# Optimization experiments

Measured on AMD Instinct MI355X. Metric: run time of the kernel, lower is better.

## Reference

```python
import jax, jax.numpy as jnp
import numpy as np

B, N, DIM, H, KVAL = 16, 1024, 128, 8, 4  # b divisible by K*K=16; mask batch = B//(K*K)=1


def setup_inputs() -> dict:
    key = jax.random.key(0)
    ks = jax.random.split(key, 6)
    x = jax.random.normal(ks[0], (B, N, DIM), jnp.float32)
    mask = (jax.random.uniform(ks[1], (B // (KVAL * KVAL), N - 1)) < 0.9).astype(jnp.float32)
    maps = (jax.random.uniform(ks[2], (B, N - 1)) < 0.9).astype(jnp.float32)
    Wqkv = jax.random.normal(ks[3], (DIM, 3 * DIM), jnp.float32) / np.sqrt(DIM)
    Wout = jax.random.normal(ks[4], (DIM, DIM), jnp.float32) / np.sqrt(DIM)
    bout = jnp.zeros((DIM,), jnp.float32)
    return {"x": x, "mask": mask, "maps": maps, "Wqkv": Wqkv, "Wout": Wout,
            "bout": bout, "K": KVAL}


def reference(x, mask, maps, Wqkv, Wout, bout, K):
    b, n, dim = x.shape
    h = H
    d = dim // h
    scale = dim ** -0.5
    qkv = x @ Wqkv                                  # [b, n, 3*dim]
    q, k, v = jnp.split(qkv, 3, axis=-1)

    def to_heads(t):
        return t.reshape(b, n, h, d).transpose(0, 2, 1, 3)  # [b, h, n, d]

    q, k, v = to_heads(q), to_heads(k), to_heads(v)
    dots = jnp.einsum('bhid,bhjd->bhij', q, k) * scale      # [b, h, n, n]
    mask_value = -jnp.finfo(dots.dtype).max

    # block mask: pad first key position with 1, broadcast over K*K batch block
    kk = K * K
    m = jnp.pad(mask, ((0, 0), (1, 0)), constant_values=1.0)  # [b//kk, n]
    dots = dots.reshape(b // kk, kk, h, n, n)
    m5 = m[:, None, None, None, :]
    dots = dots * m5 + mask_value * (1.0 - m5)
    dots = dots.reshape(b, h, n, n)

    # map mask: boolean fill per batch element
    mp = jnp.pad(maps, ((0, 0), (1, 0)), constant_values=1.0)  # [b, n]
    dots = jnp.where(mp[:, None, None, :] != 0, dots, mask_value)

    attn = jax.nn.softmax(dots, axis=-1)
    out = jnp.einsum('bhij,bhjd->bhid', attn, v)            # [b, h, n, d]
    out = out.transpose(0, 2, 1, 3).reshape(b, n, dim)      # [b, n, dim]
    return out @ Wout + bout
```

## Files before the change

### kernel.cpp

```cpp
#include <hip/hip_runtime.h>
#include <math.h>

#define B_   16
#define N_   1024
#define DIM_ 128
#define H_   8
#define D_   16
#define BH_  128

typedef unsigned short u16;
typedef unsigned int   u32;
typedef __attribute__((ext_vector_type(8))) short short8;
typedef __attribute__((ext_vector_type(4))) float f32x4;

__device__ __forceinline__ u16 f2bf(float f) {
    union { float f; u32 i; } c; c.f = f;
    u32 r = c.i + 0x7FFFu + ((c.i >> 16) & 1u);
    return (u16)(r >> 16);
}
__device__ __forceinline__ u32 pack2bf(float a, float b) {
    union { float f; u32 i; } ca, cb; ca.f = a; cb.f = b;
    return ((ca.i + 0x8000u) >> 16) | ((cb.i + 0x8000u) & 0xFFFF0000u);
}
union frag8 { short8 s; u32 w[4]; };

#define BF_ONE  ((short)0x3F80)
#define BF_NINF ((u16)0xFF80)
#define SCALE_L2E (0.08838834764831845f * 1.4426950408889634f)
#define MFMA16 __builtin_amdgcn_mfma_f32_16x16x32_bf16

__global__ __launch_bounds__(256) void qkv_kernel(
    const float* __restrict__ x, const float* __restrict__ Wqkv,
    const float* __restrict__ maskp, const float* __restrict__ mapsp,
    u16* __restrict__ qws, u16* __restrict__ kws2, u16* __restrict__ vtws)
{
    const int tid  = threadIdx.x;
    const int wave = tid >> 6, lane = tid & 63;
    const int i16  = lane & 15, quad = lane >> 4;
    const int cb   = blockIdx.x % 6;
    const int rb   = blockIdx.x / 6;
    const int row_m = rb * 64 + wave * 16;

    const float* xp = x + (size_t)(row_m + i16) * 128;

    short8 a0, a1, a2, a3;
    #define LOADA(A, K0) { \
        const int k0 = (K0) + quad * 8; \
        const float4 xa = *(const float4*)(xp + k0); \
        const float4 xb2 = *(const float4*)(xp + k0 + 4); \
        frag8 t_; \
        t_.w[0] = pack2bf(xa.x, xa.y);  t_.w[1] = pack2bf(xa.z, xa.w); \
        t_.w[2] = pack2bf(xb2.x, xb2.y); t_.w[3] = pack2bf(xb2.z, xb2.w); \
        A = t_.s; }
    LOADA(a0, 0) LOADA(a1, 32) LOADA(a2, 64) LOADA(a3, 96)
    #undef LOADA

    f32x4 acc0 = {0,0,0,0}, acc1 = {0,0,0,0}, acc2 = {0,0,0,0}, acc3 = {0,0,0,0};

    #define KSTEP(A, K0) { \
        const int k0 = (K0) + quad * 8; \
        const float* wk = Wqkv + (size_t)k0 * 384 + cb * 64 + i16; \
        _Pragma("unroll") \
        for (int ct = 0; ct < 4; ct++) { \
            const float* wp = wk + ct * 16; \
            const float w0 = wp[0*384], w1 = wp[1*384], w2 = wp[2*384], w3 = wp[3*384]; \
            const float w4 = wp[4*384], w5 = wp[5*384], w6 = wp[6*384], w7 = wp[7*384]; \
            frag8 b_; \
            b_.w[0] = pack2bf(w0, w1); b_.w[1] = pack2bf(w2, w3); \
            b_.w[2] = pack2bf(w4, w5); b_.w[3] = pack2bf(w6, w7); \
            if      (ct == 0) acc0 = MFMA16(A, b_.s, acc0, 0, 0, 0); \
            else if (ct == 1) acc1 = MFMA16(A, b_.s, acc1, 0, 0, 0); \
            else if (ct == 2) acc2 = MFMA16(A, b_.s, acc2, 0, 0, 0); \
            else              acc3 = MFMA16(A, b_.s, acc3, 0, 0, 0); \
        } }
    KSTEP(a0, 0) KSTEP(a1, 32) KSTEP(a2, 64) KSTEP(a3, 96)
    #undef KSTEP

    const int which = (cb * 64) >> 7;
    const int row   = row_m + quad * 4;
    const int bb    = row >> 10, n = row & 1023;

    #define STORE_CT(CT, ACC) { \
        const int c  = (cb * 64 + CT * 16) & 127; \
        const int h  = c >> 4; \
        const int bh = bb * 8 + h; \
        const int dd = i16; \
        if (which == 0) { \
            u16* p = qws + ((size_t)(bh * N_ + n)) * 16 + dd; \
            p[0]  = f2bf(ACC[0] * SCALE_L2E); p[16] = f2bf(ACC[1] * SCALE_L2E); \
            p[32] = f2bf(ACC[2] * SCALE_L2E); p[48] = f2bf(ACC[3] * SCALE_L2E); \
        } else if (which == 1) { \
            u16* p = kws2 + ((size_t)(bh * N_ + n)) * 32 + dd; \
            p[0]  = f2bf(ACC[0]); p[32] = f2bf(ACC[1]); \
            p[64] = f2bf(ACC[2]); p[96] = f2bf(ACC[3]); \
            if (dd == 0) { \
                _Pragma("unroll") \
                for (int r = 0; r < 4; r++) { \
                    const int nr = n + r; \
                    const bool valid = (nr == 0) || \
                        (maskp[nr - 1] != 0.0f && mapsp[bb * (N_ - 1) + nr - 1] != 0.0f); \
                    kws2[((size_t)(bh * N_ + nr)) * 32 + 16] = valid ? (u16)0 : BF_NINF; \
                } \
            } \
        } else { \
            *(ushort4*)(vtws + ((size_t)(bh * 16 + dd)) * N_ + n) = \
                make_ushort4(f2bf(ACC[0]), f2bf(ACC[1]), f2bf(ACC[2]), f2bf(ACC[3])); \
        } }
    STORE_CT(0, acc0)
    STORE_CT(1, acc1)
    STORE_CT(2, acc2)
    STORE_CT(3, acc3)
    #undef STORE_CT
}

__global__ __launch_bounds__(256) void attn_kernel(
    const u16* __restrict__ qws, const u16* __restrict__ kws2, const u16* __restrict__ vtws,
    u16* __restrict__ attn)
{
    const int tid  = threadIdx.x;
    const int wave = tid >> 6, lane = tid & 63;
    const int i16  = lane & 15, quad = lane >> 4;
    const int bh   = blockIdx.x;
    const int qb   = blockIdx.y;
    const int bb   = bh >> 3, h = bh & 7;
    const int qrow0 = qb * 256 + wave * 64;
    const int perm = ((i16 & 12) << 1) | (i16 & 3);

    const short8 zero8 = {0,0,0,0,0,0,0,0};
    const short8 ones8 = {BF_ONE,BF_ONE,BF_ONE,BF_ONE,BF_ONE,BF_ONE,BF_ONE,BF_ONE};

    short8 qf0 = zero8, qf1 = zero8, qf2 = zero8, qf3 = zero8;
    if (lane < 32) {
        const u16* qp = qws + ((size_t)(bh * N_ + qrow0 + i16)) * 16 + quad * 8;
        qf0 = *(const short8*)(qp);
        qf1 = *(const short8*)(qp + 256);
        qf2 = *(const short8*)(qp + 512);
        qf3 = *(const short8*)(qp + 768);
    } else if (lane < 48) {
        qf0[0] = BF_ONE; qf1[0] = BF_ONE; qf2[0] = BF_ONE; qf3[0] = BF_ONE;
    }

    const u16* kpA = kws2 + ((size_t)(bh * N_ + perm)) * 32 + quad * 8;
    const u16* kpB = kpA + 4 * 32;
    const u16* vp  = vtws + ((size_t)(bh * 16 + i16)) * N_ + quad * 8;

    f32x4 o0 = {0,0,0,0}, o1 = {0,0,0,0}, o2 = {0,0,0,0}, o3 = {0,0,0,0};
    f32x4 l0 = {0,0,0,0}, l1 = {0,0,0,0}, l2 = {0,0,0,0}, l3 = {0,0,0,0};
    const f32x4 zc = {0.f, 0.f, 0.f, 0.f};

    #pragma unroll 2
    for (int j0 = 0; j0 < N_; j0 += 32) {
        const short8 kfA = *(const short8*)kpA;
        const short8 kfB = *(const short8*)kpB;
        const short8 vf  = *(const short8*)vp;
        kpA += 32 * 32; kpB += 32 * 32; vp += 32;

        #define TILE(QF, O, L) { \
            f32x4 stA = MFMA16(kfA, QF, zc, 0, 0, 0); \
            f32x4 stB = MFMA16(kfB, QF, zc, 0, 0, 0); \
            float pA0 = __builtin_amdgcn_exp2f(stA[0]); \
            float pA1 = __builtin_amdgcn_exp2f(stA[1]); \
            float pA2 = __builtin_amdgcn_exp2f(stA[2]); \
            float pA3 = __builtin_amdgcn_exp2f(stA[3]); \
            float pB0 = __builtin_amdgcn_exp2f(stB[0]); \
            float pB1 = __builtin_amdgcn_exp2f(stB[1]); \
            float pB2 = __builtin_amdgcn_exp2f(stB[2]); \
            float pB3 = __builtin_amdgcn_exp2f(stB[3]); \
            frag8 pk; \
            pk.w[0] = pack2bf(pA0, pA1); pk.w[1] = pack2bf(pA2, pA3); \
            pk.w[2] = pack2bf(pB0, pB1); pk.w[3] = pack2bf(pB2, pB3); \
            O = MFMA16(vf,    pk.s, O, 0, 0, 0); \
            L = MFMA16(ones8, pk.s, L, 0, 0, 0); }
        TILE(qf0, o0, l0)
        TILE(qf1, o1, l1)
        TILE(qf2, o2, l2)
        TILE(qf3, o3, l3)
        #undef TILE
    }

    #define OUT_T(T, O, L) { \
        const float inv = 1.0f / L[0]; \
        ushort4 pko = make_ushort4(f2bf(O[0] * inv), f2bf(O[1] * inv), \
                                   f2bf(O[2] * inv), f2bf(O[3] * inv)); \
        *(ushort4*)(attn + ((size_t)(bb * N_ + qrow0 + T * 16 + i16)) * DIM_ \
                    + h * 16 + quad * 4) = pko; }
    OUT_T(0, o0, l0)
    OUT_T(1, o1, l1)
    OUT_T(2, o2, l2)
    OUT_T(3, o3, l3)
    #undef OUT_T
}

__global__ __launch_bounds__(256) void out_kernel(
    const u16* __restrict__ attnw, const float* __restrict__ Wout,
    const float* __restrict__ boutp, float* __restrict__ outp)
{
    const int tid  = threadIdx.x;
    const int wave = tid >> 6, lane = tid & 63;
    const int i16  = lane & 15, quad = lane >> 4;
    const int cb   = blockIdx.x & 1;
    const int rb   = blockIdx.x >> 1;
    const int row_m = rb * 64 + wave * 16;

    const u16* ap = attnw + (size_t)(row_m + i16) * 128;

    f32x4 acc0 = {0,0,0,0}, acc1 = {0,0,0,0}, acc2 = {0,0,0,0}, acc3 = {0,0,0,0};

    #pragma unroll
    for (int ks = 0; ks < 4; ks++) {
        const int k0 = ks * 32 + quad * 8;
        const short8 a = *(const short8*)(ap + k0);
        const float* wk = Wout + (size_t)k0 * 128 + cb * 64 + i16;
        #pragma unroll
        for (int ct = 0; ct < 4; ct++) {
            const float* wp = wk + ct * 16;
            const float w0 = wp[0*128], w1 = wp[1*128], w2 = wp[2*128], w3 = wp[3*128];
            const float w4 = wp[4*128], w5 = wp[5*128], w6 = wp[6*128], w7 = wp[7*128];
            frag8 b_;
            b_.w[0] = pack2bf(w0, w1); b_.w[1] = pack2bf(w2, w3);
            b_.w[2] = pack2bf(w4, w5); b_.w[3] = pack2bf(w6, w7);
            if      (ct == 0) acc0 = MFMA16(a, b_.s, acc0, 0, 0, 0);
            else if (ct == 1) acc1 = MFMA16(a, b_.s, acc1, 0, 0, 0);
            else if (ct == 2) acc2 = MFMA16(a, b_.s, acc2, 0, 0, 0);
            else              acc3 = MFMA16(a, b_.s, acc3, 0, 0, 0);
        }
    }

    const int row = row_m + quad * 4;
    #define STORE_CT(CT, ACC) { \
        const int col = cb * 64 + CT * 16 + i16; \
        const float bo = boutp[col]; \
        float* op = outp + (size_t)row * 128 + col; \
        op[0 * 128] = ACC[0] + bo; \
        op[1 * 128] = ACC[1] + bo; \
        op[2 * 128] = ACC[2] + bo; \
        op[3 * 128] = ACC[3] + bo; }
    STORE_CT(0, acc0)
    STORE_CT(1, acc1)
    STORE_CT(2, acc2)
    STORE_CT(3, acc3)
    #undef STORE_CT
}

extern "C" void kernel_launch(void* const* d_in, const int* in_sizes, int n_in,
                              void* d_out, int out_size, void* d_ws, size_t ws_size,
                              hipStream_t stream) {
    const float* x    = (const float*)d_in[0];
    const float* mask = (const float*)d_in[1];
    const float* maps = (const float*)d_in[2];
    const float* Wqkv = (const float*)d_in[3];
    const float* Wout = (const float*)d_in[4];
    const float* bout = (const float*)d_in[5];
    u16* qws   = (u16*)d_ws;
    u16* kws2  = qws  + (size_t)2 * 1024 * 1024;
    u16* vtws  = kws2 + (size_t)4 * 1024 * 1024;
    u16* attnw = vtws + (size_t)2 * 1024 * 1024;

    qkv_kernel<<<dim3(1536), dim3(256), 0, stream>>>(x, Wqkv, mask, maps, qws, kws2, vtws);
    attn_kernel<<<dim3(128, 4), dim3(256), 0, stream>>>(qws, kws2, vtws, attnw);
    out_kernel<<<dim3(512), dim3(256), 0, stream>>>(attnw, Wout, bout, (float*)d_out);
}
```

Baseline: 129.0 us.

## Stage bf16 weight tiles in LDS for QKV and output projections

Both projection kernels now have the block cooperatively load fp32 weights once, convert them to bf16, and store them transposed in padded shared memory. Each wave then reads its MFMA B-fragments with vector LDS loads, replacing eight strided scalar global loads and packing per fragment in every wave. The QKV kernel also makes each block cover three 64-column tiles instead of one, so a loaded x fragment is reused across more outputs and the grid shrinks from 1536 to 512 blocks. This costs a larger LDS footprint (about 52 KB in qkv) and a barrier, which may reduce occupancy and parallelism.

```diff
diff --git a/kernel.cpp b/kernel.cpp
--- a/kernel.cpp
+++ b/kernel.cpp
@@ -29,20 +29,38 @@
 #define SCALE_L2E (0.08838834764831845f * 1.4426950408889634f)
 #define MFMA16 __builtin_amdgcn_mfma_f32_16x16x32_bf16
 
+#define WSTRIDE 136
+
 __global__ __launch_bounds__(256) void qkv_kernel(
     const float* __restrict__ x, const float* __restrict__ Wqkv,
     const float* __restrict__ maskp, const float* __restrict__ mapsp,
     u16* __restrict__ qws, u16* __restrict__ kws2, u16* __restrict__ vtws)
 {
+    __shared__ u16 wlds[3 * 64 * WSTRIDE];
     const int tid  = threadIdx.x;
     const int wave = tid >> 6, lane = tid & 63;
     const int i16  = lane & 15, quad = lane >> 4;
-    const int cb   = blockIdx.x % 6;
-    const int rb   = blockIdx.x / 6;
+    const int half = blockIdx.x & 1;
+    const int rb   = blockIdx.x >> 1;
     const int row_m = rb * 64 + wave * 16;
+    const int colbase0 = half * 192;
+
+    {
+        const int col = tid & 63, pg = tid >> 6;
+        for (int ci = 0; ci < 3; ci++) {
+            const float* wsrc = Wqkv + colbase0 + ci * 64 + col;
+            u16* dst = wlds + ci * (64 * WSTRIDE) + col * WSTRIDE;
+            #pragma unroll
+            for (int it = 0; it < 16; it++) {
+                const int p = it * 4 + pg;
+                const float v0 = wsrc[(size_t)(2 * p)     * 384];
+                const float v1 = wsrc[(size_t)(2 * p + 1) * 384];
+                *(u32*)(dst + 2 * p) = pack2bf(v0, v1);
+            }
+        }
+    }
 
     const float* xp = x + (size_t)(row_m + i16) * 128;
-
     short8 a0, a1, a2, a3;
     #define LOADA(A, K0) { \
         const int k0 = (K0) + quad * 8; \
@@ -55,62 +73,59 @@
     LOADA(a0, 0) LOADA(a1, 32) LOADA(a2, 64) LOADA(a3, 96)
     #undef LOADA
 
-    f32x4 acc0 = {0,0,0,0}, acc1 = {0,0,0,0}, acc2 = {0,0,0,0}, acc3 = {0,0,0,0};
-
-    #define KSTEP(A, K0) { \
-        const int k0 = (K0) + quad * 8; \
-        const float* wk = Wqkv + (size_t)k0 * 384 + cb * 64 + i16; \
-        _Pragma("unroll") \
-        for (int ct = 0; ct < 4; ct++) { \
-            const float* wp = wk + ct * 16; \
-            const float w0 = wp[0*384], w1 = wp[1*384], w2 = wp[2*384], w3 = wp[3*384]; \
-            const float w4 = wp[4*384], w5 = wp[5*384], w6 = wp[6*384], w7 = wp[7*384]; \
-            frag8 b_; \
-            b_.w[0] = pack2bf(w0, w1); b_.w[1] = pack2bf(w2, w3); \
-            b_.w[2] = pack2bf(w4, w5); b_.w[3] = pack2bf(w6, w7); \
-            if      (ct == 0) acc0 = MFMA16(A, b_.s, acc0, 0, 0, 0); \
-            else if (ct == 1) acc1 = MFMA16(A, b_.s, acc1, 0, 0, 0); \
-            else if (ct == 2) acc2 = MFMA16(A, b_.s, acc2, 0, 0, 0); \
-            else              acc3 = MFMA16(A, b_.s, acc3, 0, 0, 0); \
-        } }
-    KSTEP(a0, 0) KSTEP(a1, 32) KSTEP(a2, 64) KSTEP(a3, 96)
-    #undef KSTEP
-
-    const int which = (cb * 64) >> 7;
-    const int row   = row_m + quad * 4;
-    const int bb    = row >> 10, n = row & 1023;
-
-    #define STORE_CT(CT, ACC) { \
-        const int c  = (cb * 64 + CT * 16) & 127; \
-        const int h  = c >> 4; \
-        const int bh = bb * 8 + h; \
-        const int dd = i16; \
-        if (which == 0) { \
-            u16* p = qws + ((size_t)(bh * N_ + n)) * 16 + dd; \
-            p[0]  = f2bf(ACC[0] * SCALE_L2E); p[16] = f2bf(ACC[1] * SCALE_L2E); \
-            p[32] = f2bf(ACC[2] * SCALE_L2E); p[48] = f2bf(ACC[3] * SCALE_L2E); \
-        } else if (which == 1) { \
-            u16* p = kws2 + ((size_t)(bh * N_ + n)) * 32 + dd; \
-            p[0]  = f2bf(ACC[0]); p[32] = f2bf(ACC[1]); \
-            p[64] = f2bf(ACC[2]); p[96] = f2bf(ACC[3]); \
-            if (dd == 0) { \
-                _Pragma("unroll") \
-                for (int r = 0; r < 4; r++) { \
-                    const int nr = n + r; \
-                    const bool valid = (nr == 0) || \
-                        (maskp[nr - 1] != 0.0f && mapsp[bb * (N_ - 1) + nr - 1] != 0.0f); \
-                    kws2[((size_t)(bh * N_ + nr)) * 32 + 16] = valid ? (u16)0 : BF_NINF; \
+    __syncthreads();
+
+    const int row = row_m + quad * 4;
+    const int bb  = row >> 10, n = row & 1023;
+
+    #pragma unroll 1
+    for (int ci = 0; ci < 3; ci++) {
+        const int cb = half * 3 + ci;
+        const u16* wt = wlds + ci * (64 * WSTRIDE);
+        f32x4 acc0 = {0,0,0,0}, acc1 = {0,0,0,0}, acc2 = {0,0,0,0}, acc3 = {0,0,0,0};
+
+        #define KSTEP(A, K0) { \
+            const int k0 = (K0) + quad * 8; \
+            acc0 = MFMA16(A, *(const short8*)(wt + (0*16 + i16) * WSTRIDE + k0), acc0, 0,0,0); \
+            acc1 = MFMA16(A, *(const short8*)(wt + (1*16 + i16) * WSTRIDE + k0), acc1, 0,0,0); \
+            acc2 = MFMA16(A, *(const short8*)(wt + (2*16 + i16) * WSTRIDE + k0), acc2, 0,0,0); \
+            acc3 = MFMA16(A, *(const short8*)(wt + (3*16 + i16) * WSTRIDE + k0), acc3, 0,0,0); }
+        KSTEP(a0, 0) KSTEP(a1, 32) KSTEP(a2, 64) KSTEP(a3, 96)
+        #undef KSTEP
+
+        const int which = (cb * 64) >> 7;
+        #define STORE_CT(CT, ACC) { \
+            const int c  = (cb * 64 + CT * 16) & 127; \
+            const int h  = c >> 4; \
+            const int bh = bb * 8 + h; \
+            const int dd = i16; \
+            if (which == 0) { \
+                u16* p = qws + ((size_t)(bh * N_ + n)) * 16 + dd; \
+                p[0]  = f2bf(ACC[0] * SCALE_L2E); p[16] = f2bf(ACC[1] * SCALE_L2E); \
+                p[32] = f2bf(ACC[2] * SCALE_L2E); p[48] = f2bf(ACC[3] * SCALE_L2E); \
+            } else if (which == 1) { \
+                u16* p = kws2 + ((size_t)(bh * N_ + n)) * 32 + dd; \
+                p[0]  = f2bf(ACC[0]); p[32] = f2bf(ACC[1]); \
+                p[64] = f2bf(ACC[2]); p[96] = f2bf(ACC[3]); \
+                if (dd == 0) { \
+                    _Pragma("unroll") \
+                    for (int r = 0; r < 4; r++) { \
+                        const int nr = n + r; \
+                        const bool valid = (nr == 0) || \
+                            (maskp[nr - 1] != 0.0f && mapsp[bb * (N_ - 1) + nr - 1] != 0.0f); \
+                        kws2[((size_t)(bh * N_ + nr)) * 32 + 16] = valid ? (u16)0 : BF_NINF; \
+                    } \
                 } \
-            } \
-        } else { \
-            *(ushort4*)(vtws + ((size_t)(bh * 16 + dd)) * N_ + n) = \
-                make_ushort4(f2bf(ACC[0]), f2bf(ACC[1]), f2bf(ACC[2]), f2bf(ACC[3])); \
-        } }
-    STORE_CT(0, acc0)
-    STORE_CT(1, acc1)
-    STORE_CT(2, acc2)
-    STORE_CT(3, acc3)
-    #undef STORE_CT
+            } else { \
+                *(ushort4*)(vtws + ((size_t)(bh * 16 + dd)) * N_ + n) = \
+                    make_ushort4(f2bf(ACC[0]), f2bf(ACC[1]), f2bf(ACC[2]), f2bf(ACC[3])); \
+            } }
+        STORE_CT(0, acc0)
+        STORE_CT(1, acc1)
+        STORE_CT(2, acc2)
+        STORE_CT(3, acc3)
+        #undef STORE_CT
+    }
 }
 
 __global__ __launch_bounds__(256) void attn_kernel(
@@ -195,6 +210,7 @@
     const u16* __restrict__ attnw, const float* __restrict__ Wout,
     const float* __restrict__ boutp, float* __restrict__ outp)
 {
+    __shared__ u16 wlds[64 * WSTRIDE];
     const int tid  = threadIdx.x;
     const int wave = tid >> 6, lane = tid & 63;
     const int i16  = lane & 15, quad = lane >> 4;
@@ -202,29 +218,36 @@
     const int rb   = blockIdx.x >> 1;
     const int row_m = rb * 64 + wave * 16;
 
+    {
+        const int col = tid & 63, pg = tid >> 6;
+        const float* wsrc = Wout + cb * 64 + col;
+        u16* dst = wlds + col * WSTRIDE;
+        #pragma unroll
+        for (int it = 0; it < 16; it++) {
+            const int p = it * 4 + pg;
+            const float v0 = wsrc[(size_t)(2 * p)     * 128];
+            const float v1 = wsrc[(size_t)(2 * p + 1) * 128];
+            *(u32*)(dst + 2 * p) = pack2bf(v0, v1);
+        }
+    }
+
     const u16* ap = attnw + (size_t)(row_m + i16) * 128;
+    short8 a0 = *(const short8*)(ap + quad * 8);
+    short8 a1 = *(const short8*)(ap + 32 + quad * 8);
+    short8 a2 = *(const short8*)(ap + 64 + quad * 8);
+    short8 a3 = *(const short8*)(ap + 96 + quad * 8);
+
+    __syncthreads();
 
     f32x4 acc0 = {0,0,0,0}, acc1 = {0,0,0,0}, acc2 = {0,0,0,0}, acc3 = {0,0,0,0};
-
-    #pragma unroll
-    for (int ks = 0; ks < 4; ks++) {
-        const int k0 = ks * 32 + quad * 8;
-        const short8 a = *(const short8*)(ap + k0);
-        const float* wk = Wout + (size_t)k0 * 128 + cb * 64 + i16;
-        #pragma unroll
-        for (int ct = 0; ct < 4; ct++) {
-            const float* wp = wk + ct * 16;
-            const float w0 = wp[0*128], w1 = wp[1*128], w2 = wp[2*128], w3 = wp[3*128];
-            const float w4 = wp[4*128], w5 = wp[5*128], w6 = wp[6*128], w7 = wp[7*128];
-            frag8 b_;
-            b_.w[0] = pack2bf(w0, w1); b_.w[1] = pack2bf(w2, w3);
-            b_.w[2] = pack2bf(w4, w5); b_.w[3] = pack2bf(w6, w7);
-            if      (ct == 0) acc0 = MFMA16(a, b_.s, acc0, 0, 0, 0);
-            else if (ct == 1) acc1 = MFMA16(a, b_.s, acc1, 0, 0, 0);
-            else if (ct == 2) acc2 = MFMA16(a, b_.s, acc2, 0, 0, 0);
-            else              acc3 = MFMA16(a, b_.s, acc3, 0, 0, 0);
-        }
-    }
+    #define KSTEP(A, K0) { \
+        const int k0 = (K0) + quad * 8; \
+        acc0 = MFMA16(A, *(const short8*)(wlds + (0*16 + i16) * WSTRIDE + k0), acc0, 0,0,0); \
+        acc1 = MFMA16(A, *(const short8*)(wlds + (1*16 + i16) * WSTRIDE + k0), acc1, 0,0,0); \
+        acc2 = MFMA16(A, *(const short8*)(wlds + (2*16 + i16) * WSTRIDE + k0), acc2, 0,0,0); \
+        acc3 = MFMA16(A, *(const short8*)(wlds + (3*16 + i16) * WSTRIDE + k0), acc3, 0,0,0); }
+    KSTEP(a0, 0) KSTEP(a1, 32) KSTEP(a2, 64) KSTEP(a3, 96)
+    #undef KSTEP
 
     const int row = row_m + quad * 4;
     #define STORE_CT(CT, ACC) { \
@@ -256,7 +279,7 @@
     u16* vtws  = kws2 + (size_t)4 * 1024 * 1024;
     u16* attnw = vtws + (size_t)2 * 1024 * 1024;
 
-    qkv_kernel<<<dim3(1536), dim3(256), 0, stream>>>(x, Wqkv, mask, maps, qws, kws2, vtws);
+    qkv_kernel<<<dim3(512), dim3(256), 0, stream>>>(x, Wqkv, mask, maps, qws, kws2, vtws);
     attn_kernel<<<dim3(128, 4), dim3(256), 0, stream>>>(qws, kws2, vtws, attnw);
     out_kernel<<<dim3(512), dim3(256), 0, stream>>>(attnw, Wout, bout, (float*)d_out);
 }
```

Result: faster. 120.6 us (-6.5%).
